# Optimization experiments

Measured on AMD Instinct MI355X. Metric: run time of the kernel, lower is better.

Reference implementation:

```python
import jax, jax.numpy as jnp
import numpy as np
from jax import lax

N_TRACES = 128
TRACE_LEN = 32          # uniform trace length -> seq_len
INPUT_DIM = 64
HIDDEN_DIM = 128
BATCH = N_TRACES * TRACE_LEN  # 4096 events = batch_size


def setup_inputs() -> dict:
    key = jax.random.key(0)
    ks = jax.random.split(key, 12)
    s = 1.0 / np.sqrt(HIDDEN_DIM)
    u = lambda k, shape: jax.random.uniform(k, shape, jnp.float32, -s, s)
    return {
        "input": jax.random.normal(ks[0], (BATCH, INPUT_DIM), jnp.float32),
        # layer 0 LSTM params (gate order i,f,g,o as in torch)
        "W_ih0": u(ks[1], (4 * HIDDEN_DIM, INPUT_DIM)),
        "W_hh0": u(ks[2], (4 * HIDDEN_DIM, HIDDEN_DIM)),
        "b_ih0": u(ks[3], (4 * HIDDEN_DIM,)),
        "b_hh0": u(ks[4], (4 * HIDDEN_DIM,)),
        # layer 1 LSTM params
        "W_ih1": u(ks[5], (4 * HIDDEN_DIM, HIDDEN_DIM)),
        "W_hh1": u(ks[6], (4 * HIDDEN_DIM, HIDDEN_DIM)),
        "b_ih1": u(ks[7], (4 * HIDDEN_DIM,)),
        "b_hh1": u(ks[8], (4 * HIDDEN_DIM,)),
        # final linear: hidden -> 1
        "W_lin": u(ks[9], (1, HIDDEN_DIM)),
        "b_lin": u(ks[10], (1,)),
    }


def _lstm_layer(xs, W_ih, W_hh, b_ih, b_hh):
    # xs: [T, B, D_in] time-major. Returns hidden stream [T, B, H].
    H = W_hh.shape[1]
    B = xs.shape[1]
    # precompute input projection for all timesteps
    x_proj = jnp.einsum('tbd,gd->tbg', xs, W_ih) + b_ih + b_hh  # [T,B,4H]

    def step(carry, xp):
        h, c = carry
        gates = xp + h @ W_hh.T                # [B,4H]
        i, f, g, o = jnp.split(gates, 4, axis=-1)
        i = jax.nn.sigmoid(i)
        f = jax.nn.sigmoid(f)
        g = jnp.tanh(g)
        o = jax.nn.sigmoid(o)
        c = f * c + i * g
        h = o * jnp.tanh(c)
        return (h, c), h

    h0 = jnp.zeros((B, H), xs.dtype)
    _, hs = lax.scan(step, (h0, h0), x_proj)
    return hs


def _forward(input, W_ih0, W_hh0, b_ih0, b_hh0, W_ih1, W_hh1, b_ih1, b_hh1, W_lin, b_lin):
    L, D = TRACE_LEN, INPUT_DIM
    # Prefix scatter: event k of a trace gets the padded prefix events[0..k].
    x_tr = input.reshape(N_TRACES, L, D)                       # [Ntr, L, D]
    causal = (jnp.arange(L)[None, :] <= jnp.arange(L)[:, None])  # [k, j] mask j<=k
    padded = x_tr[:, None, :, :] * causal[None, :, :, None].astype(input.dtype)  # [Ntr,L(k),L(j),D]
    padded = padded.reshape(BATCH, L, D)                       # batch-first padded sequences

    xs = jnp.transpose(padded, (1, 0, 2))                      # [L, B, D] time-major
    h1 = _lstm_layer(xs, W_ih0, W_hh0, b_ih0, b_hh0)           # [L, B, H]
    h2 = _lstm_layer(h1, W_ih1, W_hh1, b_ih1, b_hh1)           # [L, B, H]

    out = jnp.einsum('tbh,oh->tbo', h2, W_lin) + b_lin         # [L, B, 1]
    # last valid timestep gather: lengths[i]-1 = (i mod L)
    lens_m1 = jnp.tile(jnp.arange(L), N_TRACES)                # [B]
    y_pred = out[lens_m1, jnp.arange(BATCH), 0]                # [B]
    return y_pred


def reference(input, W_ih0, W_hh0, b_ih0, b_hh0, W_ih1, W_hh1, b_ih1, b_hh1, W_lin, b_lin):
    return _forward(input, W_ih0, W_hh0, b_ih0, b_hh0, W_ih1, W_hh1, b_ih1, b_hh1, W_lin, b_lin)
```

## Files before the change

kernel.cpp:

```cpp
#include <hip/hip_runtime.h>

#define N_TRACES 128
#define TLEN 32
#define IN_DIM 64
#define HID 128
#define G4 (4 * HID)
#define BATCH (N_TRACES * TLEN)


__device__ __forceinline__ float fast_sigmoid(float x) {
    return 1.0f / (1.0f + __expf(-x));
}
__device__ __forceinline__ float fast_tanh(float x) {
    return 1.0f - 2.0f / (__expf(2.0f * x) + 1.0f);
}
__device__ __forceinline__ float quad_reduce(float x) {
    x += __int_as_float(__builtin_amdgcn_update_dpp(
        0, __float_as_int(x), 0xB1 , 0xF, 0xF, true));
    x += __int_as_float(__builtin_amdgcn_update_dpp(
        0, __float_as_int(x), 0x4E , 0xF, 0xF, true));
    return x;
}

__device__ __forceinline__ void load_w(const float* __restrict__ W, int u, int s,
                                       float (&w)[4][32]) {
    #pragma unroll
    for (int i = 0; i < 4; ++i) {
        const float* wr = W + (size_t)(u + 128 * i) * HID + 32 * s;
        #pragma unroll
        for (int j = 0; j < 8; ++j) {
            float4 v = *(const float4*)(wr + 4 * j);
            w[i][4 * j + 0] = v.x; w[i][4 * j + 1] = v.y;
            w[i][4 * j + 2] = v.z; w[i][4 * j + 3] = v.w;
        }
    }
    #pragma unroll
    for (int i = 0; i < 4; ++i)
        #pragma unroll
        for (int j = 0; j < 32; ++j)
            asm volatile("" : "+v"(w[i][j]));
}

__device__ __forceinline__ void matvec_acc(const float (&w)[4][32],
                                           const float* hb, float (&acc)[4]) {
    #pragma unroll
    for (int j = 0; j < 8; ++j) {
        float4 v = *(const float4*)(hb + 4 * j);
        float hx[4] = {v.x, v.y, v.z, v.w};
        #pragma unroll
        for (int e = 0; e < 4; ++e) {
            #pragma unroll
            for (int i = 0; i < 4; ++i)
                acc[i] = fmaf(w[i][4 * j + e], hx[e], acc[i]);
        }
    }
}


template <int K>
__global__ __launch_bounds__(256) void gemm_bt(
    const float* __restrict__ A,
    const float* __restrict__ W,
    const float* __restrict__ b1,
    const float* __restrict__ b2,
    float* __restrict__ out,
    int Nld)
{
    constexpr int LD = 68;
    __shared__ float At[K][LD];
    __shared__ float Wt[K][LD];

    const int tid = threadIdx.x;
    const int m0 = blockIdx.x * 64;
    const int n0 = blockIdx.y * 64;

    const int rot = tid & 3;
    #pragma unroll
    for (int j = 0; j < K / 16; ++j) {
        const int e = 4 * (tid + 256 * j);
        const int row = e / K;
        const int k = e % K;
        float4 va = *(const float4*)(A + (size_t)(m0 + row) * K + k);
        float4 vw = *(const float4*)(W + (size_t)(n0 + row) * K + k);
        float fa[4] = {va.x, va.y, va.z, va.w};
        float fw[4] = {vw.x, vw.y, vw.z, vw.w};
        #pragma unroll
        for (int ii = 0; ii < 4; ++ii) {
            const int i = (ii + rot) & 3;
            At[k + i][row] = fa[i];
            Wt[k + i][row] = fw[i];
        }
    }
    __syncthreads();

    const int tx = tid & 15;
    const int ty = tid >> 4;
    float acc[4][4] = {};

    #pragma unroll 4
    for (int k = 0; k < K; ++k) {
        float4 a = *(const float4*)&At[k][ty * 4];
        float4 w = *(const float4*)&Wt[k][tx * 4];
        acc[0][0] = fmaf(a.x, w.x, acc[0][0]); acc[0][1] = fmaf(a.x, w.y, acc[0][1]);
        acc[0][2] = fmaf(a.x, w.z, acc[0][2]); acc[0][3] = fmaf(a.x, w.w, acc[0][3]);
        acc[1][0] = fmaf(a.y, w.x, acc[1][0]); acc[1][1] = fmaf(a.y, w.y, acc[1][1]);
        acc[1][2] = fmaf(a.y, w.z, acc[1][2]); acc[1][3] = fmaf(a.y, w.w, acc[1][3]);
        acc[2][0] = fmaf(a.z, w.x, acc[2][0]); acc[2][1] = fmaf(a.z, w.y, acc[2][1]);
        acc[2][2] = fmaf(a.z, w.z, acc[2][2]); acc[2][3] = fmaf(a.z, w.w, acc[2][3]);
        acc[3][0] = fmaf(a.w, w.x, acc[3][0]); acc[3][1] = fmaf(a.w, w.y, acc[3][1]);
        acc[3][2] = fmaf(a.w, w.z, acc[3][2]); acc[3][3] = fmaf(a.w, w.w, acc[3][3]);
    }

    float bb[4];
    #pragma unroll
    for (int j = 0; j < 4; ++j) {
        const int n = n0 + tx * 4 + j;
        bb[j] = b1[n] + b2[n];
    }
    #pragma unroll
    for (int i = 0; i < 4; ++i) {
        const int m = m0 + ty * 4 + i;
        float4 v;
        v.x = acc[i][0] + bb[0]; v.y = acc[i][1] + bb[1];
        v.z = acc[i][2] + bb[2]; v.w = acc[i][3] + bb[3];
        *(float4*)(out + (size_t)m * Nld + n0 + tx * 4) = v;
    }
}


__global__ __launch_bounds__(512) void fused_trace(
    const float* __restrict__ xproj0,
    const float* __restrict__ Whh0,
    const float* __restrict__ Wih1,
    const float* __restrict__ bih1,
    const float* __restrict__ bhh1,
    const float* __restrict__ Whh1,
    const float* __restrict__ Wlin,
    const float* __restrict__ blin,
    float* __restrict__ y)
{
    const int trace = blockIdx.x;
    const int tid = threadIdx.x;
    const int u = tid >> 2;
    const int s = tid & 3;
    const int pu = u + 4 * (u >> 5);

    __shared__ float hs[TLEN][140];
    __shared__ float xp[TLEN * G4];

    float w[4][32];

    const float* xpb = xproj0 + (size_t)trace * TLEN * G4;
    #pragma unroll
    for (int j = 0; j < 8; ++j) {
        const int f4 = j * 512 + tid;
        float4 v = *(const float4*)(xpb + 4 * f4);
        *(float4*)(&xp[4 * f4]) = v;
    }
    load_w(Whh0, u, s, w);
    __syncthreads();

    float c = 0.0f;
    #pragma unroll 1
    for (int t = 0; t < TLEN; ++t) {
        float xg[4];
        #pragma unroll
        for (int i = 0; i < 4; ++i) xg[i] = xp[t * G4 + 128 * i + u];

        float acc[4] = {0.f, 0.f, 0.f, 0.f};
        if (t > 0) matvec_acc(w, &hs[t - 1][36 * s], acc);
        #pragma unroll
        for (int i = 0; i < 4; ++i) acc[i] = quad_reduce(acc[i]);

        if (s == 0) {
            const float iv = fast_sigmoid(acc[0] + xg[0]);
            const float fv = fast_sigmoid(acc[1] + xg[1]);
            const float gv = fast_tanh(acc[2] + xg[2]);
            const float ov = fast_sigmoid(acc[3] + xg[3]);
            c = fv * c + iv * gv;
            hs[t][pu] = ov * fast_tanh(c);
        }
        __syncthreads();
    }

    load_w(Wih1, u, s, w);
    float bi[4] = {0.f, 0.f, 0.f, 0.f};
    if (s == 0) {
        #pragma unroll
        for (int i = 0; i < 4; ++i) bi[i] = bih1[u + 128 * i] + bhh1[u + 128 * i];
    }
    #pragma unroll 1
    for (int t = 0; t < TLEN; ++t) {
        float acc[4] = {0.f, 0.f, 0.f, 0.f};
        matvec_acc(w, &hs[t][36 * s], acc);
        #pragma unroll
        for (int i = 0; i < 4; ++i) acc[i] = quad_reduce(acc[i]);
        if (s == 0) {
            #pragma unroll
            for (int i = 0; i < 4; ++i) xp[t * G4 + 128 * i + u] = acc[i] + bi[i];
        }
    }
    __syncthreads();

    load_w(Whh1, u, s, w);
    c = 0.0f;
    #pragma unroll 1
    for (int t = 0; t < TLEN; ++t) {
        float xg[4];
        #pragma unroll
        for (int i = 0; i < 4; ++i) xg[i] = xp[t * G4 + 128 * i + u];

        float acc[4] = {0.f, 0.f, 0.f, 0.f};
        if (t > 0) matvec_acc(w, &hs[t - 1][36 * s], acc);
        #pragma unroll
        for (int i = 0; i < 4; ++i) acc[i] = quad_reduce(acc[i]);

        if (s == 0) {
            const float iv = fast_sigmoid(acc[0] + xg[0]);
            const float fv = fast_sigmoid(acc[1] + xg[1]);
            const float gv = fast_tanh(acc[2] + xg[2]);
            const float ov = fast_sigmoid(acc[3] + xg[3]);
            c = fv * c + iv * gv;
            hs[t][pu] = ov * fast_tanh(c);
        }
        __syncthreads();
    }

    if (tid < 128) {
        const int tq = tid >> 2;
        const int sq = tid & 3;
        float wl[32];
        #pragma unroll
        for (int j = 0; j < 8; ++j) {
            float4 v = *(const float4*)(Wlin + 32 * sq + 4 * j);
            wl[4 * j + 0] = v.x; wl[4 * j + 1] = v.y;
            wl[4 * j + 2] = v.z; wl[4 * j + 3] = v.w;
        }
        const float* hb = &hs[tq][36 * sq];
        float a = 0.f;
        #pragma unroll
        for (int j = 0; j < 8; ++j) {
            float4 v = *(const float4*)(hb + 4 * j);
            a = fmaf(v.x, wl[4 * j + 0], a);
            a = fmaf(v.y, wl[4 * j + 1], a);
            a = fmaf(v.z, wl[4 * j + 2], a);
            a = fmaf(v.w, wl[4 * j + 3], a);
        }
        a = quad_reduce(a);
        if (sq == 0) y[trace * TLEN + tq] = a + blin[0];
    }
}


extern "C" void kernel_launch(void* const* d_in, const int* in_sizes, int n_in,
                              void* d_out, int out_size, void* d_ws, size_t ws_size,
                              hipStream_t stream) {
    const float* input = (const float*)d_in[0];
    const float* W_ih0 = (const float*)d_in[1];
    const float* W_hh0 = (const float*)d_in[2];
    const float* b_ih0 = (const float*)d_in[3];
    const float* b_hh0 = (const float*)d_in[4];
    const float* W_ih1 = (const float*)d_in[5];
    const float* W_hh1 = (const float*)d_in[6];
    const float* b_ih1 = (const float*)d_in[7];
    const float* b_hh1 = (const float*)d_in[8];
    const float* W_lin = (const float*)d_in[9];
    const float* b_lin = (const float*)d_in[10];
    float* out = (float*)d_out;

    float* xproj0 = (float*)d_ws;

    dim3 ggrid(BATCH / 64, G4 / 64);

    gemm_bt<IN_DIM><<<ggrid, 256, 0, stream>>>(input, W_ih0, b_ih0, b_hh0, xproj0, G4);
    fused_trace<<<N_TRACES, 512, 0, stream>>>(xproj0, W_hh0, W_ih1, b_ih1, b_hh1,
                                              W_hh1, W_lin, b_lin, out);
}
```

Before: 168.3 us.

## Split LSTM hidden matvec across 8 lanes with 1024-thread blocks

The fused per-trace LSTM kernel now splits each hidden unit's dot product across 8 lanes instead of 4, and uses 1024 threads per block. Each thread holds 16 weights per gate instead of 32, so the serial FMA chain per timestep is halved; a third DPP step (row half-mirror) finishes the 8-lane reduction. All lanes now compute the gate nonlinearities redundantly, which removes the lane divergence, and the shared hidden-state row is re-padded to 20-float segments. The cost is more waves taking part in each per-timestep barrier and one extra cross-lane reduction step.

```diff
diff --git a/kernel.cpp b/kernel.cpp
--- a/kernel.cpp
+++ b/kernel.cpp
@@ -6,6 +6,7 @@
 #define HID 128
 #define G4 (4 * HID)
 #define BATCH (N_TRACES * TLEN)
+#define HROW 160
 
 
 __device__ __forceinline__ float fast_sigmoid(float x) {
@@ -14,21 +15,23 @@
 __device__ __forceinline__ float fast_tanh(float x) {
     return 1.0f - 2.0f / (__expf(2.0f * x) + 1.0f);
 }
-__device__ __forceinline__ float quad_reduce(float x) {
+__device__ __forceinline__ float oct_reduce(float x) {
     x += __int_as_float(__builtin_amdgcn_update_dpp(
         0, __float_as_int(x), 0xB1 , 0xF, 0xF, true));
     x += __int_as_float(__builtin_amdgcn_update_dpp(
         0, __float_as_int(x), 0x4E , 0xF, 0xF, true));
+    x += __int_as_float(__builtin_amdgcn_update_dpp(
+        0, __float_as_int(x), 0x141 , 0xF, 0xF, true));
     return x;
 }
 
-__device__ __forceinline__ void load_w(const float* __restrict__ W, int u, int s,
-                                       float (&w)[4][32]) {
+__device__ __forceinline__ void load_w16(const float* __restrict__ W, int u, int s,
+                                         float (&w)[4][16]) {
     #pragma unroll
     for (int i = 0; i < 4; ++i) {
-        const float* wr = W + (size_t)(u + 128 * i) * HID + 32 * s;
-        #pragma unroll
-        for (int j = 0; j < 8; ++j) {
+        const float* wr = W + (size_t)(u + 128 * i) * HID + 16 * s;
+        #pragma unroll
+        for (int j = 0; j < 4; ++j) {
             float4 v = *(const float4*)(wr + 4 * j);
             w[i][4 * j + 0] = v.x; w[i][4 * j + 1] = v.y;
             w[i][4 * j + 2] = v.z; w[i][4 * j + 3] = v.w;
@@ -37,14 +40,14 @@
     #pragma unroll
     for (int i = 0; i < 4; ++i)
         #pragma unroll
-        for (int j = 0; j < 32; ++j)
+        for (int j = 0; j < 16; ++j)
             asm volatile("" : "+v"(w[i][j]));
 }
 
-__device__ __forceinline__ void matvec_acc(const float (&w)[4][32],
-                                           const float* hb, float (&acc)[4]) {
-    #pragma unroll
-    for (int j = 0; j < 8; ++j) {
+__device__ __forceinline__ void matvec_acc16(const float (&w)[4][16],
+                                             const float* hb, float (&acc)[4]) {
+    #pragma unroll
+    for (int j = 0; j < 4; ++j) {
         float4 v = *(const float4*)(hb + 4 * j);
         float hx[4] = {v.x, v.y, v.z, v.w};
         #pragma unroll
@@ -128,7 +131,7 @@
 }
 
 
-__global__ __launch_bounds__(512) void fused_trace(
+__global__ __launch_bounds__(1024) void fused_trace(
     const float* __restrict__ xproj0,
     const float* __restrict__ Whh0,
     const float* __restrict__ Wih1,
@@ -141,23 +144,22 @@
 {
     const int trace = blockIdx.x;
     const int tid = threadIdx.x;
-    const int u = tid >> 2;
-    const int s = tid & 3;
-    const int pu = u + 4 * (u >> 5);
-
-    __shared__ float hs[TLEN][140];
-    __shared__ float xp[TLEN * G4];
-
-    float w[4][32];
+    const int u = tid >> 3;
+    const int s = tid & 7;
+    const int hw = 20 * (u >> 4) + (u & 15);
+
+    __shared__ __align__(16) float hs[TLEN][HROW];
+    __shared__ __align__(16) float xp[TLEN * G4];
+
+    float w[4][16];
 
     const float* xpb = xproj0 + (size_t)trace * TLEN * G4;
     #pragma unroll
-    for (int j = 0; j < 8; ++j) {
-        const int f4 = j * 512 + tid;
-        float4 v = *(const float4*)(xpb + 4 * f4);
-        *(float4*)(&xp[4 * f4]) = v;
-    }
-    load_w(Whh0, u, s, w);
+    for (int j = 0; j < 4; ++j) {
+        const int f4 = j * 1024 + tid;
+        *(float4*)(&xp[4 * f4]) = *(const float4*)(xpb + 4 * f4);
+    }
+    load_w16(Whh0, u, s, w);
     __syncthreads();
 
     float c = 0.0f;
@@ -168,33 +170,30 @@
         for (int i = 0; i < 4; ++i) xg[i] = xp[t * G4 + 128 * i + u];
 
         float acc[4] = {0.f, 0.f, 0.f, 0.f};
-        if (t > 0) matvec_acc(w, &hs[t - 1][36 * s], acc);
-        #pragma unroll
-        for (int i = 0; i < 4; ++i) acc[i] = quad_reduce(acc[i]);
-
-        if (s == 0) {
-            const float iv = fast_sigmoid(acc[0] + xg[0]);
-            const float fv = fast_sigmoid(acc[1] + xg[1]);
-            const float gv = fast_tanh(acc[2] + xg[2]);
-            const float ov = fast_sigmoid(acc[3] + xg[3]);
-            c = fv * c + iv * gv;
-            hs[t][pu] = ov * fast_tanh(c);
-        }
+        if (t > 0) matvec_acc16(w, &hs[t - 1][20 * s], acc);
+        #pragma unroll
+        for (int i = 0; i < 4; ++i) acc[i] = oct_reduce(acc[i]);
+
+        const float iv = fast_sigmoid(acc[0] + xg[0]);
+        const float fv = fast_sigmoid(acc[1] + xg[1]);
+        const float gv = fast_tanh(acc[2] + xg[2]);
+        const float ov = fast_sigmoid(acc[3] + xg[3]);
+        c = fv * c + iv * gv;
+        const float h = ov * fast_tanh(c);
+        if (s == 0) hs[t][hw] = h;
         __syncthreads();
     }
 
-    load_w(Wih1, u, s, w);
-    float bi[4] = {0.f, 0.f, 0.f, 0.f};
-    if (s == 0) {
-        #pragma unroll
-        for (int i = 0; i < 4; ++i) bi[i] = bih1[u + 128 * i] + bhh1[u + 128 * i];
-    }
+    load_w16(Wih1, u, s, w);
+    float bi[4];
+    #pragma unroll
+    for (int i = 0; i < 4; ++i) bi[i] = bih1[u + 128 * i] + bhh1[u + 128 * i];
     #pragma unroll 1
     for (int t = 0; t < TLEN; ++t) {
         float acc[4] = {0.f, 0.f, 0.f, 0.f};
-        matvec_acc(w, &hs[t][36 * s], acc);
-        #pragma unroll
-        for (int i = 0; i < 4; ++i) acc[i] = quad_reduce(acc[i]);
+        matvec_acc16(w, &hs[t][20 * s], acc);
+        #pragma unroll
+        for (int i = 0; i < 4; ++i) acc[i] = oct_reduce(acc[i]);
         if (s == 0) {
             #pragma unroll
             for (int i = 0; i < 4; ++i) xp[t * G4 + 128 * i + u] = acc[i] + bi[i];
@@ -202,7 +201,7 @@
     }
     __syncthreads();
 
-    load_w(Whh1, u, s, w);
+    load_w16(Whh1, u, s, w);
     c = 0.0f;
     #pragma unroll 1
     for (int t = 0; t < TLEN; ++t) {
@@ -211,42 +210,41 @@
         for (int i = 0; i < 4; ++i) xg[i] = xp[t * G4 + 128 * i + u];
 
         float acc[4] = {0.f, 0.f, 0.f, 0.f};
-        if (t > 0) matvec_acc(w, &hs[t - 1][36 * s], acc);
-        #pragma unroll
-        for (int i = 0; i < 4; ++i) acc[i] = quad_reduce(acc[i]);
-
-        if (s == 0) {
-            const float iv = fast_sigmoid(acc[0] + xg[0]);
-            const float fv = fast_sigmoid(acc[1] + xg[1]);
-            const float gv = fast_tanh(acc[2] + xg[2]);
-            const float ov = fast_sigmoid(acc[3] + xg[3]);
-            c = fv * c + iv * gv;
-            hs[t][pu] = ov * fast_tanh(c);
-        }
+        if (t > 0) matvec_acc16(w, &hs[t - 1][20 * s], acc);
+        #pragma unroll
+        for (int i = 0; i < 4; ++i) acc[i] = oct_reduce(acc[i]);
+
+        const float iv = fast_sigmoid(acc[0] + xg[0]);
+        const float fv = fast_sigmoid(acc[1] + xg[1]);
+        const float gv = fast_tanh(acc[2] + xg[2]);
+        const float ov = fast_sigmoid(acc[3] + xg[3]);
+        c = fv * c + iv * gv;
+        const float h = ov * fast_tanh(c);
+        if (s == 0) hs[t][hw] = h;
         __syncthreads();
     }
 
-    if (tid < 128) {
-        const int tq = tid >> 2;
-        const int sq = tid & 3;
-        float wl[32];
-        #pragma unroll
-        for (int j = 0; j < 8; ++j) {
-            float4 v = *(const float4*)(Wlin + 32 * sq + 4 * j);
+    if (tid < 256) {
+        const int tq = tid >> 3;
+        const int sq = tid & 7;
+        float wl[16];
+        #pragma unroll
+        for (int j = 0; j < 4; ++j) {
+            float4 v = *(const float4*)(Wlin + 16 * sq + 4 * j);
             wl[4 * j + 0] = v.x; wl[4 * j + 1] = v.y;
             wl[4 * j + 2] = v.z; wl[4 * j + 3] = v.w;
         }
-        const float* hb = &hs[tq][36 * sq];
+        const float* hb = &hs[tq][20 * sq];
         float a = 0.f;
         #pragma unroll
-        for (int j = 0; j < 8; ++j) {
+        for (int j = 0; j < 4; ++j) {
             float4 v = *(const float4*)(hb + 4 * j);
             a = fmaf(v.x, wl[4 * j + 0], a);
             a = fmaf(v.y, wl[4 * j + 1], a);
             a = fmaf(v.z, wl[4 * j + 2], a);
             a = fmaf(v.w, wl[4 * j + 3], a);
         }
-        a = quad_reduce(a);
+        a = oct_reduce(a);
         if (sq == 0) y[trace * TLEN + tq] = a + blin[0];
     }
 }
@@ -273,6 +271,6 @@
     dim3 ggrid(BATCH / 64, G4 / 64);
 
     gemm_bt<IN_DIM><<<ggrid, 256, 0, stream>>>(input, W_ih0, b_ih0, b_hh0, xproj0, G4);
-    fused_trace<<<N_TRACES, 512, 0, stream>>>(xproj0, W_hh0, W_ih1, b_ih1, b_hh1,
-                                              W_hh1, W_lin, b_lin, out);
-}
+    fused_trace<<<N_TRACES, 1024, 0, stream>>>(xproj0, W_hh0, W_ih1, b_ih1, b_hh1,
+                                               W_hh1, W_lin, b_lin, out);
+}
```

Measured after the change: 180.5 us. 7.2% more time.

## Batch 16 traces per block and run LSTM recurrences on bf16 MFMA with split precision

Applied to the files above, without the earlier changes.

Rewrites the fused recurrent kernel so each block processes 16 traces at once, computing the hidden-state matvecs as 16x16x32 bf16 MFMA tiles. fp32 accuracy is approximated by splitting weights and hidden states into hi/lo bf16 parts and issuing three MFMAs per chunk. Hidden streams and the layer-1 input projection are spilled to global workspace instead of shared memory, and the next step's gate inputs are prefetched into registers. This cuts the grid from 128 blocks to 8, trading parallelism across CUs for tensor-core throughput. It also adds global memory traffic and introduces a small precision loss.

```diff
diff --git a/kernel.cpp b/kernel.cpp
--- a/kernel.cpp
+++ b/kernel.cpp
@@ -6,6 +6,12 @@
 #define HID 128
 #define G4 (4 * HID)
 #define BATCH (N_TRACES * TLEN)
+#define TPB 16
+#define NBLK (N_TRACES / TPB)
+#define HPAD 136
+
+typedef float f32x4 __attribute__((ext_vector_type(4)));
+typedef __bf16 bf16x8 __attribute__((ext_vector_type(8)));
 
 
 __device__ __forceinline__ float fast_sigmoid(float x) {
@@ -13,47 +19,6 @@
 }
 __device__ __forceinline__ float fast_tanh(float x) {
     return 1.0f - 2.0f / (__expf(2.0f * x) + 1.0f);
-}
-__device__ __forceinline__ float quad_reduce(float x) {
-    x += __int_as_float(__builtin_amdgcn_update_dpp(
-        0, __float_as_int(x), 0xB1 , 0xF, 0xF, true));
-    x += __int_as_float(__builtin_amdgcn_update_dpp(
-        0, __float_as_int(x), 0x4E , 0xF, 0xF, true));
-    return x;
-}
-
-__device__ __forceinline__ void load_w(const float* __restrict__ W, int u, int s,
-                                       float (&w)[4][32]) {
-    #pragma unroll
-    for (int i = 0; i < 4; ++i) {
-        const float* wr = W + (size_t)(u + 128 * i) * HID + 32 * s;
-        #pragma unroll
-        for (int j = 0; j < 8; ++j) {
-            float4 v = *(const float4*)(wr + 4 * j);
-            w[i][4 * j + 0] = v.x; w[i][4 * j + 1] = v.y;
-            w[i][4 * j + 2] = v.z; w[i][4 * j + 3] = v.w;
-        }
-    }
-    #pragma unroll
-    for (int i = 0; i < 4; ++i)
-        #pragma unroll
-        for (int j = 0; j < 32; ++j)
-            asm volatile("" : "+v"(w[i][j]));
-}
-
-__device__ __forceinline__ void matvec_acc(const float (&w)[4][32],
-                                           const float* hb, float (&acc)[4]) {
-    #pragma unroll
-    for (int j = 0; j < 8; ++j) {
-        float4 v = *(const float4*)(hb + 4 * j);
-        float hx[4] = {v.x, v.y, v.z, v.w};
-        #pragma unroll
-        for (int e = 0; e < 4; ++e) {
-            #pragma unroll
-            for (int i = 0; i < 4; ++i)
-                acc[i] = fmaf(w[i][4 * j + e], hx[e], acc[i]);
-        }
-    }
 }
 
 
@@ -128,7 +93,83 @@
 }
 
 
-__global__ __launch_bounds__(512) void fused_trace(
+__device__ __forceinline__ void load_wfrag(const float* __restrict__ W, int u, int q,
+                                           bf16x8 (&bh)[4][4], bf16x8 (&bl)[4][4])
+{
+    #pragma unroll
+    for (int gi = 0; gi < 4; ++gi) {
+        const float* wr = W + (size_t)(u + 128 * gi) * HID + 8 * q;
+        #pragma unroll
+        for (int kc = 0; kc < 4; ++kc) {
+            float4 v0 = *(const float4*)(wr + 32 * kc);
+            float4 v1 = *(const float4*)(wr + 32 * kc + 4);
+            float f0[4] = {v0.x, v0.y, v0.z, v0.w};
+            float f1[4] = {v1.x, v1.y, v1.z, v1.w};
+            bf16x8 h, l;
+            #pragma unroll
+            for (int e = 0; e < 4; ++e) {
+                __bf16 t0 = (__bf16)f0[e];
+                h[e] = t0; l[e] = (__bf16)(f0[e] - (float)t0);
+                __bf16 t1 = (__bf16)f1[e];
+                h[4 + e] = t1; l[4 + e] = (__bf16)(f1[e] - (float)t1);
+            }
+            bh[gi][kc] = h; bl[gi][kc] = l;
+        }
+    }
+}
+
+__device__ __forceinline__ void matstep(
+    const __bf16 (&shi)[TPB][HPAD], const __bf16 (&slo)[TPB][HPAD],
+    const bf16x8 (&bh)[4][4], const bf16x8 (&bl)[4][4],
+    int cl, int q, f32x4 (&acc)[4])
+{
+    bf16x8 ah[4], al[4];
+    #pragma unroll
+    for (int kc = 0; kc < 4; ++kc) {
+        ah[kc] = *(const bf16x8*)&shi[cl][32 * kc + 8 * q];
+        al[kc] = *(const bf16x8*)&slo[cl][32 * kc + 8 * q];
+    }
+    #pragma unroll
+    for (int gi = 0; gi < 4; ++gi) {
+        #pragma unroll
+        for (int kc = 0; kc < 4; ++kc) {
+            acc[gi] = __builtin_amdgcn_mfma_f32_16x16x32_bf16(ah[kc], bh[gi][kc], acc[gi], 0, 0, 0);
+            acc[gi] = __builtin_amdgcn_mfma_f32_16x16x32_bf16(al[kc], bh[gi][kc], acc[gi], 0, 0, 0);
+            acc[gi] = __builtin_amdgcn_mfma_f32_16x16x32_bf16(ah[kc], bl[gi][kc], acc[gi], 0, 0, 0);
+        }
+    }
+}
+
+__device__ __forceinline__ void gate_stage(
+    const f32x4 (&acc)[4], const f32x4 (&xg)[4], const float (&bias)[4],
+    float (&cst)[4], int q, int u,
+    __bf16 (&shi)[TPB][HPAD], __bf16 (&slo)[TPB][HPAD],
+    __bf16* __restrict__ dhi, __bf16* __restrict__ dlo)
+{
+    #pragma unroll
+    for (int r = 0; r < 4; ++r) {
+        const int m = 4 * q + r;
+        const float gI = acc[0][r] + xg[0][r] + bias[0];
+        const float gF = acc[1][r] + xg[1][r] + bias[1];
+        const float gG = acc[2][r] + xg[2][r] + bias[2];
+        const float gO = acc[3][r] + xg[3][r] + bias[3];
+        const float iv = fast_sigmoid(gI);
+        const float fv = fast_sigmoid(gF);
+        const float gv = fast_tanh(gG);
+        const float ov = fast_sigmoid(gO);
+        cst[r] = fv * cst[r] + iv * gv;
+        const float h = ov * fast_tanh(cst[r]);
+        const __bf16 hb = (__bf16)h;
+        const __bf16 lb = (__bf16)(h - (float)hb);
+        shi[m][u] = hb;
+        slo[m][u] = lb;
+        dhi[(size_t)m * HID + u] = hb;
+        dlo[(size_t)m * HID + u] = lb;
+    }
+}
+
+
+__global__ __launch_bounds__(512, 2) void fused_mfma(
     const float* __restrict__ xproj0,
     const float* __restrict__ Whh0,
     const float* __restrict__ Wih1,
@@ -137,117 +178,166 @@
     const float* __restrict__ Whh1,
     const float* __restrict__ Wlin,
     const float* __restrict__ blin,
+    float* __restrict__ xp1d,
+    __bf16* __restrict__ h1hi,
+    __bf16* __restrict__ h1lo,
+    __bf16* __restrict__ h2hi,
+    __bf16* __restrict__ h2lo,
     float* __restrict__ y)
 {
-    const int trace = blockIdx.x;
+    const int b = blockIdx.x;
     const int tid = threadIdx.x;
-    const int u = tid >> 2;
-    const int s = tid & 3;
-    const int pu = u + 4 * (u >> 5);
-
-    __shared__ float hs[TLEN][140];
-    __shared__ float xp[TLEN * G4];
-
-    float w[4][32];
-
-    const float* xpb = xproj0 + (size_t)trace * TLEN * G4;
-    #pragma unroll
-    for (int j = 0; j < 8; ++j) {
-        const int f4 = j * 512 + tid;
-        float4 v = *(const float4*)(xpb + 4 * f4);
-        *(float4*)(&xp[4 * f4]) = v;
-    }
-    load_w(Whh0, u, s, w);
+    const int w = tid >> 6;
+    const int lane = tid & 63;
+    const int cl = lane & 15;
+    const int q = lane >> 4;
+    const int u = 16 * w + cl;
+
+    __shared__ __align__(16) __bf16 Shi[2][TPB][HPAD];
+    __shared__ __align__(16) __bf16 Slo[2][TPB][HPAD];
+
+    const size_t hob = (size_t)b * TLEN * TPB * HID;
+    __bf16* h1hi_b = h1hi + hob;
+    __bf16* h1lo_b = h1lo + hob;
+    __bf16* h2hi_b = h2hi + hob;
+    __bf16* h2lo_b = h2lo + hob;
+    float* xp1_b = xp1d + (size_t)b * TLEN * 8192;
+
+    bf16x8 bh[4][4], bl[4][4];
+    const float zb[4] = {0.f, 0.f, 0.f, 0.f};
+
+    const float* xb[4];
+    #pragma unroll
+    for (int r = 0; r < 4; ++r)
+        xb[r] = xproj0 + (size_t)(16 * b + 4 * q + r) * TLEN * G4 + u;
+
+    load_wfrag(Whh0, u, q, bh, bl);
+
+    f32x4 xgc[4], xgn[4];
+    #pragma unroll
+    for (int gi = 0; gi < 4; ++gi)
+        #pragma unroll
+        for (int r = 0; r < 4; ++r)
+            xgc[gi][r] = xb[r][128 * gi];
+
+    float cst[4] = {0.f, 0.f, 0.f, 0.f};
+    {
+        f32x4 accz[4] = {};
+        gate_stage(accz, xgc, zb, cst, q, u, Shi[0], Slo[0], h1hi_b, h1lo_b);
+    }
+    #pragma unroll
+    for (int gi = 0; gi < 4; ++gi)
+        #pragma unroll
+        for (int r = 0; r < 4; ++r)
+            xgn[gi][r] = xb[r][(size_t)1 * G4 + 128 * gi];
     __syncthreads();
 
-    float c = 0.0f;
+    #pragma unroll 1
+    for (int t = 1; t < TLEN; ++t) {
+        #pragma unroll
+        for (int gi = 0; gi < 4; ++gi) xgc[gi] = xgn[gi];
+        if (t < TLEN - 1) {
+            #pragma unroll
+            for (int gi = 0; gi < 4; ++gi)
+                #pragma unroll
+                for (int r = 0; r < 4; ++r)
+                    xgn[gi][r] = xb[r][(size_t)(t + 1) * G4 + 128 * gi];
+        }
+        f32x4 acc[4] = {};
+        matstep(Shi[(t - 1) & 1], Slo[(t - 1) & 1], bh, bl, cl, q, acc);
+        gate_stage(acc, xgc, zb, cst, q, u, Shi[t & 1], Slo[t & 1],
+                   h1hi_b + (size_t)t * TPB * HID, h1lo_b + (size_t)t * TPB * HID);
+        __syncthreads();
+    }
+
+    load_wfrag(Wih1, u, q, bh, bl);
     #pragma unroll 1
     for (int t = 0; t < TLEN; ++t) {
-        float xg[4];
-        #pragma unroll
-        for (int i = 0; i < 4; ++i) xg[i] = xp[t * G4 + 128 * i + u];
-
-        float acc[4] = {0.f, 0.f, 0.f, 0.f};
-        if (t > 0) matvec_acc(w, &hs[t - 1][36 * s], acc);
-        #pragma unroll
-        for (int i = 0; i < 4; ++i) acc[i] = quad_reduce(acc[i]);
-
-        if (s == 0) {
-            const float iv = fast_sigmoid(acc[0] + xg[0]);
-            const float fv = fast_sigmoid(acc[1] + xg[1]);
-            const float gv = fast_tanh(acc[2] + xg[2]);
-            const float ov = fast_sigmoid(acc[3] + xg[3]);
-            c = fv * c + iv * gv;
-            hs[t][pu] = ov * fast_tanh(c);
-        }
+        const __bf16* ph = h1hi_b + ((size_t)t * TPB + cl) * HID + 8 * q;
+        const __bf16* pl = h1lo_b + ((size_t)t * TPB + cl) * HID + 8 * q;
+        bf16x8 ah[4], al[4];
+        #pragma unroll
+        for (int kc = 0; kc < 4; ++kc) {
+            ah[kc] = *(const bf16x8*)(ph + 32 * kc);
+            al[kc] = *(const bf16x8*)(pl + 32 * kc);
+        }
+        f32x4 acc[4] = {};
+        #pragma unroll
+        for (int gi = 0; gi < 4; ++gi) {
+            #pragma unroll
+            for (int kc = 0; kc < 4; ++kc) {
+                acc[gi] = __builtin_amdgcn_mfma_f32_16x16x32_bf16(ah[kc], bh[gi][kc], acc[gi], 0, 0, 0);
+                acc[gi] = __builtin_amdgcn_mfma_f32_16x16x32_bf16(al[kc], bh[gi][kc], acc[gi], 0, 0, 0);
+                acc[gi] = __builtin_amdgcn_mfma_f32_16x16x32_bf16(ah[kc], bl[gi][kc], acc[gi], 0, 0, 0);
+            }
+        }
+        float* po = xp1_b + ((size_t)t * 8 + w) * 1024 + lane * 4;
+        #pragma unroll
+        for (int gi = 0; gi < 4; ++gi)
+            *(f32x4*)(po + gi * 256) = acc[gi];
+    }
+    __syncthreads();
+
+    load_wfrag(Whh1, u, q, bh, bl);
+    float bias[4];
+    #pragma unroll
+    for (int gi = 0; gi < 4; ++gi)
+        bias[gi] = bih1[u + 128 * gi] + bhh1[u + 128 * gi];
+
+    const float* po_base = xp1_b + w * 1024 + lane * 4;
+    f32x4 xpc[4], xpn[4];
+    #pragma unroll
+    for (int gi = 0; gi < 4; ++gi)
+        xpc[gi] = *(const f32x4*)(po_base + gi * 256);
+
+    cst[0] = cst[1] = cst[2] = cst[3] = 0.f;
+    {
+        f32x4 accz[4] = {};
+        gate_stage(accz, xpc, bias, cst, q, u, Shi[0], Slo[0], h2hi_b, h2lo_b);
+    }
+    #pragma unroll
+    for (int gi = 0; gi < 4; ++gi)
+        xpn[gi] = *(const f32x4*)(po_base + (size_t)1 * 8192 + gi * 256);
+    __syncthreads();
+
+    #pragma unroll 1
+    for (int t = 1; t < TLEN; ++t) {
+        #pragma unroll
+        for (int gi = 0; gi < 4; ++gi) xpc[gi] = xpn[gi];
+        if (t < TLEN - 1) {
+            #pragma unroll
+            for (int gi = 0; gi < 4; ++gi)
+                xpn[gi] = *(const f32x4*)(po_base + (size_t)(t + 1) * 8192 + gi * 256);
+        }
+        f32x4 acc[4] = {};
+        matstep(Shi[(t - 1) & 1], Slo[(t - 1) & 1], bh, bl, cl, q, acc);
+        gate_stage(acc, xpc, bias, cst, q, u, Shi[t & 1], Slo[t & 1],
+                   h2hi_b + (size_t)t * TPB * HID, h2lo_b + (size_t)t * TPB * HID);
         __syncthreads();
     }
 
-    load_w(Wih1, u, s, w);
-    float bi[4] = {0.f, 0.f, 0.f, 0.f};
-    if (s == 0) {
-        #pragma unroll
-        for (int i = 0; i < 4; ++i) bi[i] = bih1[u + 128 * i] + bhh1[u + 128 * i];
-    }
-    #pragma unroll 1
-    for (int t = 0; t < TLEN; ++t) {
-        float acc[4] = {0.f, 0.f, 0.f, 0.f};
-        matvec_acc(w, &hs[t][36 * s], acc);
-        #pragma unroll
-        for (int i = 0; i < 4; ++i) acc[i] = quad_reduce(acc[i]);
-        if (s == 0) {
-            #pragma unroll
-            for (int i = 0; i < 4; ++i) xp[t * G4 + 128 * i + u] = acc[i] + bi[i];
-        }
-    }
-    __syncthreads();
-
-    load_w(Whh1, u, s, w);
-    c = 0.0f;
-    #pragma unroll 1
-    for (int t = 0; t < TLEN; ++t) {
-        float xg[4];
-        #pragma unroll
-        for (int i = 0; i < 4; ++i) xg[i] = xp[t * G4 + 128 * i + u];
-
-        float acc[4] = {0.f, 0.f, 0.f, 0.f};
-        if (t > 0) matvec_acc(w, &hs[t - 1][36 * s], acc);
-        #pragma unroll
-        for (int i = 0; i < 4; ++i) acc[i] = quad_reduce(acc[i]);
-
-        if (s == 0) {
-            const float iv = fast_sigmoid(acc[0] + xg[0]);
-            const float fv = fast_sigmoid(acc[1] + xg[1]);
-            const float gv = fast_tanh(acc[2] + xg[2]);
-            const float ov = fast_sigmoid(acc[3] + xg[3]);
-            c = fv * c + iv * gv;
-            hs[t][pu] = ov * fast_tanh(c);
-        }
-        __syncthreads();
-    }
-
-    if (tid < 128) {
-        const int tq = tid >> 2;
-        const int sq = tid & 3;
-        float wl[32];
-        #pragma unroll
-        for (int j = 0; j < 8; ++j) {
-            float4 v = *(const float4*)(Wlin + 32 * sq + 4 * j);
-            wl[4 * j + 0] = v.x; wl[4 * j + 1] = v.y;
-            wl[4 * j + 2] = v.z; wl[4 * j + 3] = v.w;
-        }
-        const float* hb = &hs[tq][36 * sq];
+    {
+        const int t = tid >> 4;
+        const int tr = tid & 15;
+        const __bf16* ph = h2hi_b + ((size_t)t * TPB + tr) * HID;
+        const __bf16* pl = h2lo_b + ((size_t)t * TPB + tr) * HID;
         float a = 0.f;
         #pragma unroll
-        for (int j = 0; j < 8; ++j) {
-            float4 v = *(const float4*)(hb + 4 * j);
-            a = fmaf(v.x, wl[4 * j + 0], a);
-            a = fmaf(v.y, wl[4 * j + 1], a);
-            a = fmaf(v.z, wl[4 * j + 2], a);
-            a = fmaf(v.w, wl[4 * j + 3], a);
-        }
-        a = quad_reduce(a);
-        if (sq == 0) y[trace * TLEN + tq] = a + blin[0];
+        for (int j = 0; j < 16; ++j) {
+            bf16x8 vh = *(const bf16x8*)(ph + 8 * j);
+            bf16x8 vl = *(const bf16x8*)(pl + 8 * j);
+            float4 w0 = *(const float4*)(Wlin + 8 * j);
+            float4 w1 = *(const float4*)(Wlin + 8 * j + 4);
+            a = fmaf((float)vh[0] + (float)vl[0], w0.x, a);
+            a = fmaf((float)vh[1] + (float)vl[1], w0.y, a);
+            a = fmaf((float)vh[2] + (float)vl[2], w0.z, a);
+            a = fmaf((float)vh[3] + (float)vl[3], w0.w, a);
+            a = fmaf((float)vh[4] + (float)vl[4], w1.x, a);
+            a = fmaf((float)vh[5] + (float)vl[5], w1.y, a);
+            a = fmaf((float)vh[6] + (float)vl[6], w1.z, a);
+            a = fmaf((float)vh[7] + (float)vl[7], w1.w, a);
+        }
+        y[(size_t)(16 * b + tr) * TLEN + t] = a + blin[0];
     }
 }
 
@@ -268,11 +358,17 @@
     const float* b_lin = (const float*)d_in[10];
     float* out = (float*)d_out;
 
-    float* xproj0 = (float*)d_ws;
+    float*  xproj0 = (float*)d_ws;
+    float*  xp1d   = (float*)((char*)d_ws + (size_t)(8 << 20));
+    __bf16* h1hi   = (__bf16*)((char*)d_ws + (size_t)(16 << 20));
+    __bf16* h1lo   = (__bf16*)((char*)d_ws + (size_t)(17 << 20));
+    __bf16* h2hi   = (__bf16*)((char*)d_ws + (size_t)(18 << 20));
+    __bf16* h2lo   = (__bf16*)((char*)d_ws + (size_t)(19 << 20));
 
     dim3 ggrid(BATCH / 64, G4 / 64);
 
     gemm_bt<IN_DIM><<<ggrid, 256, 0, stream>>>(input, W_ih0, b_ih0, b_hh0, xproj0, G4);
-    fused_trace<<<N_TRACES, 512, 0, stream>>>(xproj0, W_hh0, W_ih1, b_ih1, b_hh1,
-                                              W_hh1, W_lin, b_lin, out);
-}
+    fused_mfma<<<NBLK, 512, 0, stream>>>(xproj0, W_hh0, W_ih1, b_ih1, b_hh1,
+                                         W_hh1, W_lin, b_lin,
+                                         xp1d, h1hi, h1lo, h2hi, h2lo, out);
+}
```

After: 322.4 us. 1.91x slower.

## Process two traces per block with interleaved recurrences and global xproj staging

Applied to the files above, without the earlier changes.

The fused LSTM kernel now handles two traces per block, running both recurrences in the same loop. This shares weight loads and barriers between two independent dependency chains and adds instruction-level parallelism. Input projections are read directly from global memory instead of being staged in LDS, and the layer-1 projection is written to a global workspace buffer. The t=0 step is peeled out. In exchange the grid shrinks to 64 blocks, a small fraction of the CUs, and each block does twice the FMA work per step, so the per-block critical path grows.

```diff
diff --git a/kernel.cpp b/kernel.cpp
--- a/kernel.cpp
+++ b/kernel.cpp
@@ -20,6 +20,15 @@
     x += __int_as_float(__builtin_amdgcn_update_dpp(
         0, __float_as_int(x), 0x4E , 0xF, 0xF, true));
     return x;
+}
+__device__ __forceinline__ float lstm_gate(const float (&acc)[4], const float (&xg)[4],
+                                           float& c) {
+    const float iv = fast_sigmoid(acc[0] + xg[0]);
+    const float fv = fast_sigmoid(acc[1] + xg[1]);
+    const float gv = fast_tanh(acc[2] + xg[2]);
+    const float ov = fast_sigmoid(acc[3] + xg[3]);
+    c = fv * c + iv * gv;
+    return ov * fast_tanh(c);
 }
 
 __device__ __forceinline__ void load_w(const float* __restrict__ W, int u, int s,
@@ -128,7 +137,7 @@
 }
 
 
-__global__ __launch_bounds__(512) void fused_trace(
+__global__ __launch_bounds__(512) void fused2(
     const float* __restrict__ xproj0,
     const float* __restrict__ Whh0,
     const float* __restrict__ Wih1,
@@ -137,48 +146,52 @@
     const float* __restrict__ Whh1,
     const float* __restrict__ Wlin,
     const float* __restrict__ blin,
+    float* __restrict__ xp1,
     float* __restrict__ y)
 {
-    const int trace = blockIdx.x;
+    const int trA = 2 * blockIdx.x;
     const int tid = threadIdx.x;
     const int u = tid >> 2;
     const int s = tid & 3;
     const int pu = u + 4 * (u >> 5);
 
-    __shared__ float hs[TLEN][140];
-    __shared__ float xp[TLEN * G4];
+    __shared__ __align__(16) float hs[2][TLEN][140];
 
     float w[4][32];
-
-    const float* xpb = xproj0 + (size_t)trace * TLEN * G4;
-    #pragma unroll
-    for (int j = 0; j < 8; ++j) {
-        const int f4 = j * 512 + tid;
-        float4 v = *(const float4*)(xpb + 4 * f4);
-        *(float4*)(&xp[4 * f4]) = v;
-    }
     load_w(Whh0, u, s, w);
-    __syncthreads();
-
-    float c = 0.0f;
+
+    const float* xA = xproj0 + (size_t)trA * TLEN * G4 + u;
+    const float* xB = xA + (size_t)TLEN * G4;
+
+    float cA = 0.0f, cB = 0.0f;
+    {
+        float xga[4], xgb[4];
+        #pragma unroll
+        for (int i = 0; i < 4; ++i) { xga[i] = xA[128 * i]; xgb[i] = xB[128 * i]; }
+        if (s == 0) {
+            const float za[4] = {0.f, 0.f, 0.f, 0.f};
+            hs[0][0][pu] = lstm_gate(za, xga, cA);
+            hs[1][0][pu] = lstm_gate(za, xgb, cB);
+        }
+        __syncthreads();
+    }
     #pragma unroll 1
-    for (int t = 0; t < TLEN; ++t) {
-        float xg[4];
-        #pragma unroll
-        for (int i = 0; i < 4; ++i) xg[i] = xp[t * G4 + 128 * i + u];
-
-        float acc[4] = {0.f, 0.f, 0.f, 0.f};
-        if (t > 0) matvec_acc(w, &hs[t - 1][36 * s], acc);
-        #pragma unroll
-        for (int i = 0; i < 4; ++i) acc[i] = quad_reduce(acc[i]);
-
-        if (s == 0) {
-            const float iv = fast_sigmoid(acc[0] + xg[0]);
-            const float fv = fast_sigmoid(acc[1] + xg[1]);
-            const float gv = fast_tanh(acc[2] + xg[2]);
-            const float ov = fast_sigmoid(acc[3] + xg[3]);
-            c = fv * c + iv * gv;
-            hs[t][pu] = ov * fast_tanh(c);
+    for (int t = 1; t < TLEN; ++t) {
+        float xga[4], xgb[4];
+        #pragma unroll
+        for (int i = 0; i < 4; ++i) {
+            xga[i] = xA[(size_t)t * G4 + 128 * i];
+            xgb[i] = xB[(size_t)t * G4 + 128 * i];
+        }
+        float accA[4] = {0.f, 0.f, 0.f, 0.f};
+        float accB[4] = {0.f, 0.f, 0.f, 0.f};
+        matvec_acc(w, &hs[0][t - 1][36 * s], accA);
+        matvec_acc(w, &hs[1][t - 1][36 * s], accB);
+        #pragma unroll
+        for (int i = 0; i < 4; ++i) { accA[i] = quad_reduce(accA[i]); accB[i] = quad_reduce(accB[i]); }
+        if (s == 0) {
+            hs[0][t][pu] = lstm_gate(accA, xga, cA);
+            hs[1][t][pu] = lstm_gate(accB, xgb, cB);
         }
         __syncthreads();
     }
@@ -189,46 +202,67 @@
         #pragma unroll
         for (int i = 0; i < 4; ++i) bi[i] = bih1[u + 128 * i] + bhh1[u + 128 * i];
     }
+    float* xoA = xp1 + (size_t)trA * TLEN * G4 + u;
+    float* xoB = xoA + (size_t)TLEN * G4;
     #pragma unroll 1
     for (int t = 0; t < TLEN; ++t) {
-        float acc[4] = {0.f, 0.f, 0.f, 0.f};
-        matvec_acc(w, &hs[t][36 * s], acc);
-        #pragma unroll
-        for (int i = 0; i < 4; ++i) acc[i] = quad_reduce(acc[i]);
+        float accA[4] = {0.f, 0.f, 0.f, 0.f};
+        float accB[4] = {0.f, 0.f, 0.f, 0.f};
+        matvec_acc(w, &hs[0][t][36 * s], accA);
+        matvec_acc(w, &hs[1][t][36 * s], accB);
+        #pragma unroll
+        for (int i = 0; i < 4; ++i) { accA[i] = quad_reduce(accA[i]); accB[i] = quad_reduce(accB[i]); }
         if (s == 0) {
             #pragma unroll
-            for (int i = 0; i < 4; ++i) xp[t * G4 + 128 * i + u] = acc[i] + bi[i];
+            for (int i = 0; i < 4; ++i) {
+                xoA[(size_t)t * G4 + 128 * i] = accA[i] + bi[i];
+                xoB[(size_t)t * G4 + 128 * i] = accB[i] + bi[i];
+            }
         }
     }
     __syncthreads();
 
     load_w(Whh1, u, s, w);
-    c = 0.0f;
+    const float* pA = xp1 + (size_t)trA * TLEN * G4 + u;
+    const float* pB = pA + (size_t)TLEN * G4;
+    cA = 0.0f; cB = 0.0f;
+    {
+        float xga[4], xgb[4];
+        #pragma unroll
+        for (int i = 0; i < 4; ++i) { xga[i] = pA[128 * i]; xgb[i] = pB[128 * i]; }
+        if (s == 0) {
+            const float za[4] = {0.f, 0.f, 0.f, 0.f};
+            hs[0][0][pu] = lstm_gate(za, xga, cA);
+            hs[1][0][pu] = lstm_gate(za, xgb, cB);
+        }
+        __syncthreads();
+    }
     #pragma unroll 1
-    for (int t = 0; t < TLEN; ++t) {
-        float xg[4];
-        #pragma unroll
-        for (int i = 0; i < 4; ++i) xg[i] = xp[t * G4 + 128 * i + u];
-
-        float acc[4] = {0.f, 0.f, 0.f, 0.f};
-        if (t > 0) matvec_acc(w, &hs[t - 1][36 * s], acc);
-        #pragma unroll
-        for (int i = 0; i < 4; ++i) acc[i] = quad_reduce(acc[i]);
-
-        if (s == 0) {
-            const float iv = fast_sigmoid(acc[0] + xg[0]);
-            const float fv = fast_sigmoid(acc[1] + xg[1]);
-            const float gv = fast_tanh(acc[2] + xg[2]);
-            const float ov = fast_sigmoid(acc[3] + xg[3]);
-            c = fv * c + iv * gv;
-            hs[t][pu] = ov * fast_tanh(c);
+    for (int t = 1; t < TLEN; ++t) {
+        float xga[4], xgb[4];
+        #pragma unroll
+        for (int i = 0; i < 4; ++i) {
+            xga[i] = pA[(size_t)t * G4 + 128 * i];
+            xgb[i] = pB[(size_t)t * G4 + 128 * i];
+        }
+        float accA[4] = {0.f, 0.f, 0.f, 0.f};
+        float accB[4] = {0.f, 0.f, 0.f, 0.f};
+        matvec_acc(w, &hs[0][t - 1][36 * s], accA);
+        matvec_acc(w, &hs[1][t - 1][36 * s], accB);
+        #pragma unroll
+        for (int i = 0; i < 4; ++i) { accA[i] = quad_reduce(accA[i]); accB[i] = quad_reduce(accB[i]); }
+        if (s == 0) {
+            hs[0][t][pu] = lstm_gate(accA, xga, cA);
+            hs[1][t][pu] = lstm_gate(accB, xgb, cB);
         }
         __syncthreads();
     }
 
-    if (tid < 128) {
-        const int tq = tid >> 2;
+    if (tid < 256) {
+        const int p = tid >> 2;
         const int sq = tid & 3;
+        const int m = p >> 5;
+        const int tq = p & 31;
         float wl[32];
         #pragma unroll
         for (int j = 0; j < 8; ++j) {
@@ -236,7 +270,7 @@
             wl[4 * j + 0] = v.x; wl[4 * j + 1] = v.y;
             wl[4 * j + 2] = v.z; wl[4 * j + 3] = v.w;
         }
-        const float* hb = &hs[tq][36 * sq];
+        const float* hb = &hs[m][tq][36 * sq];
         float a = 0.f;
         #pragma unroll
         for (int j = 0; j < 8; ++j) {
@@ -247,7 +281,7 @@
             a = fmaf(v.w, wl[4 * j + 3], a);
         }
         a = quad_reduce(a);
-        if (sq == 0) y[trace * TLEN + tq] = a + blin[0];
+        if (sq == 0) y[(size_t)(trA + m) * TLEN + tq] = a + blin[0];
     }
 }
 
@@ -269,10 +303,11 @@
     float* out = (float*)d_out;
 
     float* xproj0 = (float*)d_ws;
+    float* xp1    = (float*)((char*)d_ws + (size_t)(8 << 20));
 
     dim3 ggrid(BATCH / 64, G4 / 64);
 
     gemm_bt<IN_DIM><<<ggrid, 256, 0, stream>>>(input, W_ih0, b_ih0, b_hh0, xproj0, G4);
-    fused_trace<<<N_TRACES, 512, 0, stream>>>(xproj0, W_hh0, W_ih1, b_ih1, b_hh1,
-                                              W_hh1, W_lin, b_lin, out);
-}
+    fused2<<<N_TRACES / 2, 512, 0, stream>>>(xproj0, W_hh0, W_ih1, b_ih1, b_hh1,
+                                             W_hh1, W_lin, b_lin, xp1, out);
+}
```

Result: slower. 229.6 us (+36.4%).
